# Kernel tuning notes

Hardware: AMD Instinct MI355X
Metric: run time of the kernel (lower is better)

Reference implementation:

```python
import jax, jax.numpy as jnp
import numpy as np

N, E, F_NODE, F_EDGE, EMB, HID, NGRAPH = 10000, 30000, 32, 8, 64, 16, 64


def _edge_mlp(e, w1, b1, w2, b2):
    # Seq(Linear(F_EDGE,16), ReLU, Linear(16, in*out))
    return jax.nn.relu(e @ w1 + b1) @ w2 + b2


def setup_inputs() -> dict:
    key = jax.random.key(0)
    ks = jax.random.split(key, 24)
    s = lambda k, shape, fan: jax.random.normal(k, shape, jnp.float32) * (1.0 / np.sqrt(fan))
    inp = {
        "x_p": jax.random.normal(ks[0], (N, F_NODE), jnp.float32),
        "x_d": jax.random.normal(ks[1], (1, F_NODE), jnp.float32),
        "edge_attr_p": jax.random.uniform(ks[2], (E, F_EDGE), jnp.float32),
        "edge_attr_d": jax.random.uniform(ks[3], (1, F_EDGE), jnp.float32),
        "edge_index_p": jax.random.randint(ks[4], (2, E), 0, N, jnp.int32),
        "x_p_batch": jnp.sort(jax.random.randint(ks[5], (N,), 0, NGRAPH, jnp.int32)),
        # edge MLP of first conv: F_EDGE -> 16 -> F_NODE*EMB
        "nn0_w1": s(ks[6], (F_EDGE, HID), F_EDGE), "nn0_b1": jnp.zeros((HID,), jnp.float32),
        "nn0_w2": s(ks[7], (HID, F_NODE * EMB), HID), "nn0_b2": jnp.zeros((F_NODE * EMB,), jnp.float32),
        # shared edge MLP of later convs: F_EDGE -> 16 -> EMB*EMB
        "nn1_w1": s(ks[8], (F_EDGE, HID), F_EDGE), "nn1_b1": jnp.zeros((HID,), jnp.float32),
        "nn1_w2": s(ks[9], (HID, EMB * EMB), HID), "nn1_b2": jnp.zeros((EMB * EMB,), jnp.float32),
        # per-conv root weights and biases
        "root0": s(ks[10], (F_NODE, EMB), F_NODE), "bias0": jnp.zeros((EMB,), jnp.float32),
        "root1": s(ks[11], (EMB, EMB), EMB), "bias1": jnp.zeros((EMB,), jnp.float32),
        "root2": s(ks[12], (EMB, EMB), EMB), "bias2": jnp.zeros((EMB,), jnp.float32),
        # head: Linear(EMB,EMB) then Linear(EMB,1), no activation between (per source)
        "lin0_w": s(ks[13], (EMB, EMB), EMB), "lin0_b": jnp.zeros((EMB,), jnp.float32),
        "lin1_w": s(ks[14], (EMB, 1), EMB), "lin1_b": jnp.zeros((1,), jnp.float32),
    }
    return inp


def reference(x_p, x_d, edge_attr_p, edge_attr_d,
              nn0_w1, nn0_b1, nn0_w2, nn0_b2,
              nn1_w1, nn1_b1, nn1_w2, nn1_b2,
              root0, bias0, root1, bias1, root2, bias2,
              lin0_w, lin0_b, lin1_w, lin1_b,
              edge_index_p, x_p_batch):
    src, dst = edge_index_p[0], edge_index_p[1]

    # conv 0: edge-conditioned weights [E, F_NODE, EMB]
    W0 = _edge_mlp(edge_attr_p, nn0_w1, nn0_b1, nn0_w2, nn0_b2).reshape(E, F_NODE, EMB)
    msg = jnp.einsum('ei,eio->eo', x_p[src], W0)
    agg = jax.ops.segment_sum(msg, dst, num_segments=N)
    x = jax.nn.relu(agg + x_p @ root0 + bias0)

    # convs 1..L-1 share the same edge MLP (same nn1 instance in source), so
    # the per-edge weight matrices [E, EMB, EMB] are identical: compute once.
    W1 = _edge_mlp(edge_attr_p, nn1_w1, nn1_b1, nn1_w2, nn1_b2).reshape(E, EMB, EMB)
    for root, bias in ((root1, bias1), (root2, bias2)):
        msg = jnp.einsum('ei,eio->eo', x[src], W1)
        agg = jax.ops.segment_sum(msg, dst, num_segments=N)
        x = jax.nn.relu(agg + x @ root + bias)

    # global max pool over graphs, dropout is identity in eval mode
    pooled = jax.ops.segment_max(x, x_p_batch, num_segments=NGRAPH)
    h = pooled @ lin0_w + lin0_b
    out = h @ lin1_w + lin1_b  # [NGRAPH, 1]
    return out
```

## Files before the change

kernel.cpp:

```cpp
#include <hip/hip_runtime.h>
#include <hip/hip_bf16.h>

#define N_NODES 10000
#define N_EDGES 30000
#define F_NODE  32
#define F_EDGE  8
#define EMB     64
#define HID     16
#define NGRAPH  64
#define NBUCK   625
#define CAP     128
#define NCOL    1088
#define ROWW    514

typedef __attribute__((ext_vector_type(8))) short short8;
typedef __attribute__((ext_vector_type(4))) float f32x4;

__device__ __forceinline__ unsigned short f2b(float f) {
    __hip_bfloat16 h = __float2bfloat16(f);
    return __builtin_bit_cast(unsigned short, h);
}

struct P {
    const float *x_p, *ea;
    const int *src, *dst, *batch;
    const float *nn0_w1, *nn0_b1, *nn0_w2, *nn0_b2;
    const float *nn1_w1, *nn1_b1, *nn1_w2, *nn1_b2;
    const float *root0, *bias0, *root1, *bias1, *root2, *bias2;
    const float *lin0_w, *lin0_b, *lin1_w, *lin1_b;
    float *out;
    int *cursor, *metap;
    float *A0p, *A1p;
    unsigned short *W2p0, *W2p1;
    float *AGGa, *AGGb, *X0, *X1, *POOL;
};

__global__ void __launch_bounds__(256) k_prep(P p) {
    int b = blockIdx.x, t = threadIdx.x;
    if (b < 118) {
        int e = b * 256 + t;
        if (e >= N_EDGES) return;
        float f[F_EDGE];
#pragma unroll
        for (int i = 0; i < F_EDGE; i++) f[i] = p.ea[e * F_EDGE + i];
        float a0[HID], a1[HID];
#pragma unroll
        for (int h = 0; h < HID; h++) {
            float s0 = p.nn0_b1[h], s1 = p.nn1_b1[h];
#pragma unroll
            for (int i = 0; i < F_EDGE; i++) {
                s0 += f[i] * p.nn0_w1[i * HID + h];
                s1 += f[i] * p.nn1_w1[i * HID + h];
            }
            a0[h] = fmaxf(s0, 0.f);
            a1[h] = fmaxf(s1, 0.f);
        }
        int s = p.src[e];
        int bk = s >> 4;
        int pos = atomicAdd(&p.cursor[bk], 1);
        if (pos < CAP) {
            size_t base = (size_t)bk * CAP + pos;
            p.metap[base] = p.dst[e] * 16 + (s & 15);
#pragma unroll
            for (int h = 0; h < HID; h++) {
                p.A0p[base * HID + h] = a0[h];
                p.A1p[base * HID + h] = a1[h];
            }
        }
    } else if (b < 254) {
        int i = (b - 118) * 256 + t;
        if (i >= NCOL * F_NODE) return;
        int rt = i >> 5, k = i & 31;
        float v;
        if (rt < 1024) {
            int T = rt >> 4, lr = rt & 15;
            int o = ((T >> 4) << 4) + lr, h = T & 15;
            v = p.nn0_w2[h * (F_NODE * EMB) + k * EMB + o];
        } else {
            v = p.nn0_b2[k * EMB + (rt - 1024)];
        }
        p.W2p0[i] = f2b(v);
    } else if (b < 526) {
        int i = (b - 254) * 256 + t;
        if (i >= NCOL * EMB) return;
        int rt = i >> 6, k = i & 63;
        float v;
        if (rt < 1024) {
            int T = rt >> 4, lr = rt & 15;
            int o = ((T >> 4) << 4) + lr, h = T & 15;
            v = p.nn1_w2[h * (EMB * EMB) + k * EMB + o];
        } else {
            v = p.nn1_b2[k * EMB + (rt - 1024)];
        }
        p.W2p1[i] = f2b(v);
    } else {
        int idx = (b - 526) * 256 + t;
        float4* Z = (float4*)p.AGGa;
        const float4 z4 = {0.f, 0.f, 0.f, 0.f};
        for (int i = idx; i < (N_NODES * EMB + NGRAPH * EMB) / 4; i += 160 * 256)
            Z[i] = z4;
    }
}

template <int CONV>
__global__ void __launch_bounds__(512) k_fused(P p) {
    constexpr int K = (CONV == 0) ? F_NODE : EMB;
    __shared__ unsigned short U2[16 * 2 * ROWW];
    __shared__ float XB_l[16][65];
    __shared__ float Xt[16][65];
    const int b = blockIdx.x, t = threadIdx.x;
    const int n0 = b * 16;
    const int w = t >> 6, l = t & 63;
    const int lrow = l & 15, lk4 = l >> 4;

    if (CONV == 0) {
        float4* Zb = (float4*)(p.AGGb + (size_t)n0 * EMB);
        const float4 z4 = {0.f, 0.f, 0.f, 0.f};
        for (int idx = t; idx < 16 * EMB / 4; idx += 512) Zb[idx] = z4;
    }

    if (CONV > 0) {
        const float* aggIn = (CONV == 1) ? p.AGGa : p.AGGb;
        const float* rt = (CONV == 1) ? p.root0 : p.root1;
        const float* bs = (CONV == 1) ? p.bias0 : p.bias1;
        constexpr int IN = (CONV == 1) ? F_NODE : EMB;
        for (int idx = t; idx < 16 * 64; idx += 512) {
            int j = idx >> 6, o = idx & 63;
            int n = n0 + j;
            float s = aggIn[n * EMB + o] + bs[o];
            const float* xr = (CONV == 1) ? (p.x_p + (size_t)n * IN)
                                          : (p.X0 + (size_t)n * IN);
#pragma unroll
            for (int i = 0; i < IN; i++) s += xr[i] * rt[i * EMB + o];
            float sv = fmaxf(s, 0.f);
            Xt[j][o] = sv;
            if (CONV == 1) { p.X0[n * EMB + o] = sv; p.AGGa[n * EMB + o] = 0.f; }
            else           { p.X1[n * EMB + o] = sv; }
        }
        __syncthreads();
    }

    short8 afr[K / 32];
    if (CONV == 0) {
        const float* xp = p.x_p + (size_t)(n0 + lrow) * F_NODE + lk4 * 8;
#pragma unroll
        for (int q = 0; q < 8; q++) afr[0][q] = (short)f2b(xp[q]);
    } else {
#pragma unroll
        for (int kk = 0; kk < K / 32; kk++)
#pragma unroll
            for (int q = 0; q < 8; q++)
                afr[kk][q] = (short)f2b(Xt[lrow][kk * 32 + lk4 * 8 + q]);
    }
    const unsigned short* W2p = (CONV == 0) ? p.W2p0 : p.W2p1;
    for (int i = 0; i <= 8; i++) {
        int T = w + 8 * i;
        if (T >= 68) break;
        short8 bfr[K / 32];
#pragma unroll
        for (int kk = 0; kk < K / 32; kk++)
            bfr[kk] = *reinterpret_cast<const short8*>(
                W2p + (size_t)(T * 16 + lrow) * K + kk * 32 + lk4 * 8);
        f32x4 acc = {0.f, 0.f, 0.f, 0.f};
#pragma unroll
        for (int kk = 0; kk < K / 32; kk++)
            acc = __builtin_amdgcn_mfma_f32_16x16x32_bf16(afr[kk], bfr[kk], acc, 0, 0, 0);
        if (T < 64) {
            int h = T & 15, hw = h >> 1, hb = h & 1;
            int ob = ((T >> 4) << 4) + lrow;
#pragma unroll
            for (int r = 0; r < 4; r++)
                U2[(lk4 * 4 + r) * (2 * ROWW) + hw * 128 + ob * 2 + hb] = f2b(acc[r]);
        } else {
            int col = (T - 64) * 16 + lrow;
#pragma unroll
            for (int r = 0; r < 4; r++)
                XB_l[lk4 * 4 + r][col] = acc[r];
        }
    }
    __syncthreads();

    const float* Ap = (CONV == 0) ? p.A0p : p.A1p;
    float* aggOut = (CONV == 1) ? p.AGGb : p.AGGa;
    int cnt = p.cursor[b];
    if (cnt > CAP) cnt = CAP;
    const size_t base = (size_t)b * CAP;
    const int o = l;
#pragma unroll 2
    for (int qi = w; qi < cnt; qi += 8) {
        int q = __builtin_amdgcn_readfirstlane(qi);
        int mt = p.metap[base + q];
        int sloc = mt & 15, dd = mt >> 4;
        const float* Ae = Ap + (base + q) * HID;
        float av[HID];
#pragma unroll
        for (int h = 0; h < HID; h++) av[h] = Ae[h];
        const unsigned* up = reinterpret_cast<const unsigned*>(U2) + sloc * ROWW + o;
        float m = XB_l[sloc][o];
#define ACC2(wrd, h)                                                              \
        m = fmaf(__builtin_bit_cast(float, (unsigned)(wrd) << 16), av[h], m);     \
        m = fmaf(__builtin_bit_cast(float, (unsigned)(wrd) & 0xffff0000u), av[h + 1], m);
#pragma unroll
        for (int hh = 0; hh < 8; hh++) {
            unsigned uw = up[hh * 64];
            ACC2(uw, 2 * hh)
        }
#undef ACC2
        atomicAdd(&aggOut[(size_t)dd * EMB + o], m);
    }
}

__global__ void __launch_bounds__(256) k_upd2(P p) {
    int w = threadIdx.x >> 6, o = threadIdx.x & 63;
    int n = __builtin_amdgcn_readfirstlane(blockIdx.x * 4 + w);
    float s = p.AGGa[n * EMB + o] + p.bias2[o];
    const float* xr = p.X1 + (size_t)n * EMB;
#pragma unroll
    for (int i = 0; i < EMB; i++) s += xr[i] * p.root2[i * EMB + o];
    s = fmaxf(s, 0.f);
    atomicMax((unsigned*)&p.POOL[p.batch[n] * EMB + o], __float_as_uint(s));
}

__global__ void k_head(P p) {
    int g = blockIdx.x, o2 = threadIdx.x;
    float h = p.lin0_b[o2];
    const float* Pg = p.POOL + g * EMB;
    for (int o = 0; o < EMB; o++) h += Pg[o] * p.lin0_w[o * EMB + o2];
    float v = h * p.lin1_w[o2];
#pragma unroll
    for (int off = 32; off; off >>= 1) v += __shfl_down(v, off, 64);
    if (o2 == 0) p.out[g] = v + p.lin1_b[0];
}

extern "C" void kernel_launch(void* const* d_in, const int* in_sizes, int n_in,
                              void* d_out, int out_size, void* d_ws, size_t ws_size,
                              hipStream_t stream) {
    P p;
    p.x_p    = (const float*)d_in[0];
    p.ea     = (const float*)d_in[2];
    const int* eidx = (const int*)d_in[4];
    p.src    = eidx;
    p.dst    = eidx + N_EDGES;
    p.batch  = (const int*)d_in[5];
    p.nn0_w1 = (const float*)d_in[6];  p.nn0_b1 = (const float*)d_in[7];
    p.nn0_w2 = (const float*)d_in[8];  p.nn0_b2 = (const float*)d_in[9];
    p.nn1_w1 = (const float*)d_in[10]; p.nn1_b1 = (const float*)d_in[11];
    p.nn1_w2 = (const float*)d_in[12]; p.nn1_b2 = (const float*)d_in[13];
    p.root0  = (const float*)d_in[14]; p.bias0  = (const float*)d_in[15];
    p.root1  = (const float*)d_in[16]; p.bias1  = (const float*)d_in[17];
    p.root2  = (const float*)d_in[18]; p.bias2  = (const float*)d_in[19];
    p.lin0_w = (const float*)d_in[20]; p.lin0_b = (const float*)d_in[21];
    p.lin1_w = (const float*)d_in[22]; p.lin1_b = (const float*)d_in[23];
    p.out    = (float*)d_out;

    char* ws = (char*)d_ws;
    p.cursor = (int*)ws;
    p.AGGa  = (float*)(ws + 4096);
    p.POOL  = p.AGGa + (size_t)N_NODES * EMB;
    p.AGGb  = p.POOL + (size_t)NGRAPH * EMB;
    char* w2 = (char*)(p.AGGb + (size_t)N_NODES * EMB);
    p.metap = (int*)w2;            w2 += (size_t)NBUCK * CAP * 4;
    p.A0p   = (float*)w2;          w2 += (size_t)NBUCK * CAP * HID * 4;
    p.A1p   = (float*)w2;          w2 += (size_t)NBUCK * CAP * HID * 4;
    p.W2p0  = (unsigned short*)w2; w2 += (size_t)NCOL * F_NODE * 2;
    p.W2p1  = (unsigned short*)w2; w2 += (size_t)NCOL * EMB * 2;
    p.X0    = (float*)w2;          w2 += (size_t)N_NODES * EMB * 4;
    p.X1    = (float*)w2;          w2 += (size_t)N_NODES * EMB * 4;

    hipMemsetAsync(p.cursor, 0, 4096, stream);
    k_prep<<<686, 256, 0, stream>>>(p);
    k_fused<0><<<NBUCK, 512, 0, stream>>>(p);
    k_fused<1><<<NBUCK, 512, 0, stream>>>(p);
    k_fused<2><<<NBUCK, 512, 0, stream>>>(p);
    k_upd2<<<2500, 256, 0, stream>>>(p);
    k_head<<<NGRAPH, 64, 0, stream>>>(p);
}
```

Measured before the change: 211.8 us.

## Move edge bucketing and edge-MLP first layer into conv0 blocks via LDS scan

Edge bucketing by source node is no longer done with global atomics in the prep kernel followed by a memset. Each conv0 block now scans the whole src array and collects its own edges with LDS atomics. The block computes both first-layer edge MLP activations for those edges. Conv0 activations stay in LDS, and only the conv1/2 activations and metadata go to global memory. This drops the memset, the global atomic contention and the A0 round trip, but every one of the 625 blocks now reads all 30000 src indices, which is redundant global traffic.

```diff
diff --git a/kernel.cpp b/kernel.cpp
--- a/kernel.cpp
+++ b/kernel.cpp
@@ -29,46 +29,16 @@
     const float *root0, *bias0, *root1, *bias1, *root2, *bias2;
     const float *lin0_w, *lin0_b, *lin1_w, *lin1_b;
     float *out;
-    int *cursor, *metap;
-    float *A0p, *A1p;
+    int *cnt, *metap;
+    float *A1p;
     unsigned short *W2p0, *W2p1;
     float *AGGa, *AGGb, *X0, *X1, *POOL;
 };
 
 __global__ void __launch_bounds__(256) k_prep(P p) {
     int b = blockIdx.x, t = threadIdx.x;
-    if (b < 118) {
-        int e = b * 256 + t;
-        if (e >= N_EDGES) return;
-        float f[F_EDGE];
-#pragma unroll
-        for (int i = 0; i < F_EDGE; i++) f[i] = p.ea[e * F_EDGE + i];
-        float a0[HID], a1[HID];
-#pragma unroll
-        for (int h = 0; h < HID; h++) {
-            float s0 = p.nn0_b1[h], s1 = p.nn1_b1[h];
-#pragma unroll
-            for (int i = 0; i < F_EDGE; i++) {
-                s0 += f[i] * p.nn0_w1[i * HID + h];
-                s1 += f[i] * p.nn1_w1[i * HID + h];
-            }
-            a0[h] = fmaxf(s0, 0.f);
-            a1[h] = fmaxf(s1, 0.f);
-        }
-        int s = p.src[e];
-        int bk = s >> 4;
-        int pos = atomicAdd(&p.cursor[bk], 1);
-        if (pos < CAP) {
-            size_t base = (size_t)bk * CAP + pos;
-            p.metap[base] = p.dst[e] * 16 + (s & 15);
-#pragma unroll
-            for (int h = 0; h < HID; h++) {
-                p.A0p[base * HID + h] = a0[h];
-                p.A1p[base * HID + h] = a1[h];
-            }
-        }
-    } else if (b < 254) {
-        int i = (b - 118) * 256 + t;
+    if (b < 136) {
+        int i = b * 256 + t;
         if (i >= NCOL * F_NODE) return;
         int rt = i >> 5, k = i & 31;
         float v;
@@ -80,8 +50,8 @@
             v = p.nn0_b2[k * EMB + (rt - 1024)];
         }
         p.W2p0[i] = f2b(v);
-    } else if (b < 526) {
-        int i = (b - 254) * 256 + t;
+    } else if (b < 408) {
+        int i = (b - 136) * 256 + t;
         if (i >= NCOL * EMB) return;
         int rt = i >> 6, k = i & 63;
         float v;
@@ -94,11 +64,11 @@
         }
         p.W2p1[i] = f2b(v);
     } else {
-        int idx = (b - 526) * 256 + t;
+        int idx = (b - 408) * 256 + t;
         float4* Z = (float4*)p.AGGa;
         const float4 z4 = {0.f, 0.f, 0.f, 0.f};
-        for (int i = idx; i < (N_NODES * EMB + NGRAPH * EMB) / 4; i += 160 * 256)
-            Z[i] = z4;
+        const int nv4 = (N_NODES * EMB + NGRAPH * EMB) / 4;
+        for (int i = idx; i < nv4; i += 160 * 256) Z[i] = z4;
     }
 }
 
@@ -108,15 +78,60 @@
     __shared__ unsigned short U2[16 * 2 * ROWW];
     __shared__ float XB_l[16][65];
     __shared__ float Xt[16][65];
+    __shared__ float A0l[CAP][HID];
+    __shared__ int lds_e[CAP];
+    __shared__ int meta_l[CAP];
+    __shared__ int lcnt;
     const int b = blockIdx.x, t = threadIdx.x;
     const int n0 = b * 16;
     const int w = t >> 6, l = t & 63;
     const int lrow = l & 15, lk4 = l >> 4;
+    int cnt = 0;
 
     if (CONV == 0) {
         float4* Zb = (float4*)(p.AGGb + (size_t)n0 * EMB);
         const float4 z4 = {0.f, 0.f, 0.f, 0.f};
         for (int idx = t; idx < 16 * EMB / 4; idx += 512) Zb[idx] = z4;
+        if (t == 0) lcnt = 0;
+        __syncthreads();
+        const int4* s4 = (const int4*)p.src;
+        for (int i = t; i < N_EDGES / 4; i += 512) {
+            int4 v = s4[i];
+            int e0 = i * 4;
+            if ((v.x >> 4) == b) { int sl = atomicAdd(&lcnt, 1); if (sl < CAP) lds_e[sl] = ((e0    ) << 4) | (v.x & 15); }
+            if ((v.y >> 4) == b) { int sl = atomicAdd(&lcnt, 1); if (sl < CAP) lds_e[sl] = ((e0 + 1) << 4) | (v.y & 15); }
+            if ((v.z >> 4) == b) { int sl = atomicAdd(&lcnt, 1); if (sl < CAP) lds_e[sl] = ((e0 + 2) << 4) | (v.z & 15); }
+            if ((v.w >> 4) == b) { int sl = atomicAdd(&lcnt, 1); if (sl < CAP) lds_e[sl] = ((e0 + 3) << 4) | (v.w & 15); }
+        }
+        __syncthreads();
+        cnt = lcnt; if (cnt > CAP) cnt = CAP;
+        if (t == 0) p.cnt[b] = cnt;
+        if (t < cnt) {
+            int pk = lds_e[t];
+            int e = pk >> 4, sloc = pk & 15;
+            int mt = p.dst[e] * 16 + sloc;
+            meta_l[t] = mt;
+            p.metap[(size_t)b * CAP + t] = mt;
+            const float4* ea4 = (const float4*)(p.ea + (size_t)e * F_EDGE);
+            float4 ef0 = ea4[0], ef1 = ea4[1];
+            float fv[F_EDGE] = {ef0.x, ef0.y, ef0.z, ef0.w, ef1.x, ef1.y, ef1.z, ef1.w};
+            float a1v[HID];
+#pragma unroll
+            for (int h = 0; h < HID; h++) {
+                float s0 = p.nn0_b1[h], s1 = p.nn1_b1[h];
+#pragma unroll
+                for (int i = 0; i < F_EDGE; i++) {
+                    s0 += fv[i] * p.nn0_w1[i * HID + h];
+                    s1 += fv[i] * p.nn1_w1[i * HID + h];
+                }
+                A0l[t][h] = fmaxf(s0, 0.f);
+                a1v[h] = fmaxf(s1, 0.f);
+            }
+            float4* A1g = (float4*)(p.A1p + ((size_t)b * CAP + t) * HID);
+#pragma unroll
+            for (int j = 0; j < 4; j++)
+                A1g[j] = float4{a1v[4 * j], a1v[4 * j + 1], a1v[4 * j + 2], a1v[4 * j + 3]};
+        }
     }
 
     if (CONV > 0) {
@@ -138,6 +153,7 @@
             else           { p.X1[n * EMB + o] = sv; }
         }
         __syncthreads();
+        cnt = p.cnt[b];
     }
 
     short8 afr[K / 32];
@@ -180,21 +196,29 @@
     }
     __syncthreads();
 
-    const float* Ap = (CONV == 0) ? p.A0p : p.A1p;
     float* aggOut = (CONV == 1) ? p.AGGb : p.AGGa;
-    int cnt = p.cursor[b];
-    if (cnt > CAP) cnt = CAP;
     const size_t base = (size_t)b * CAP;
     const int o = l;
 #pragma unroll 2
     for (int qi = w; qi < cnt; qi += 8) {
         int q = __builtin_amdgcn_readfirstlane(qi);
-        int mt = p.metap[base + q];
+        int mt;
+        float av[HID];
+        if (CONV == 0) {
+            mt = meta_l[q];
+            const float4* a4 = (const float4*)A0l[q];
+            float4 u0 = a4[0], u1 = a4[1], u2 = a4[2], u3 = a4[3];
+            av[0]=u0.x; av[1]=u0.y; av[2]=u0.z; av[3]=u0.w;
+            av[4]=u1.x; av[5]=u1.y; av[6]=u1.z; av[7]=u1.w;
+            av[8]=u2.x; av[9]=u2.y; av[10]=u2.z; av[11]=u2.w;
+            av[12]=u3.x; av[13]=u3.y; av[14]=u3.z; av[15]=u3.w;
+        } else {
+            mt = p.metap[base + q];
+            const float* Ae = p.A1p + (base + q) * HID;
+#pragma unroll
+            for (int h = 0; h < HID; h++) av[h] = Ae[h];
+        }
         int sloc = mt & 15, dd = mt >> 4;
-        const float* Ae = Ap + (base + q) * HID;
-        float av[HID];
-#pragma unroll
-        for (int h = 0; h < HID; h++) av[h] = Ae[h];
         const unsigned* up = reinterpret_cast<const unsigned*>(U2) + sloc * ROWW + o;
         float m = XB_l[sloc][o];
 #define ACC2(wrd, h)                                                              \
@@ -254,21 +278,19 @@
     p.out    = (float*)d_out;
 
     char* ws = (char*)d_ws;
-    p.cursor = (int*)ws;
-    p.AGGa  = (float*)(ws + 4096);
-    p.POOL  = p.AGGa + (size_t)N_NODES * EMB;
-    p.AGGb  = p.POOL + (size_t)NGRAPH * EMB;
-    char* w2 = (char*)(p.AGGb + (size_t)N_NODES * EMB);
-    p.metap = (int*)w2;            w2 += (size_t)NBUCK * CAP * 4;
-    p.A0p   = (float*)w2;          w2 += (size_t)NBUCK * CAP * HID * 4;
-    p.A1p   = (float*)w2;          w2 += (size_t)NBUCK * CAP * HID * 4;
-    p.W2p0  = (unsigned short*)w2; w2 += (size_t)NCOL * F_NODE * 2;
-    p.W2p1  = (unsigned short*)w2; w2 += (size_t)NCOL * EMB * 2;
-    p.X0    = (float*)w2;          w2 += (size_t)N_NODES * EMB * 4;
-    p.X1    = (float*)w2;          w2 += (size_t)N_NODES * EMB * 4;
-
-    hipMemsetAsync(p.cursor, 0, 4096, stream);
-    k_prep<<<686, 256, 0, stream>>>(p);
+    p.AGGa   = (float*)ws;
+    p.POOL   = p.AGGa + (size_t)N_NODES * EMB;
+    char* w2 = (char*)(p.POOL + (size_t)NGRAPH * EMB);
+    p.AGGb   = (float*)w2;          w2 += (size_t)N_NODES * EMB * 4;
+    p.cnt    = (int*)w2;            w2 += 2560;
+    p.metap  = (int*)w2;            w2 += (size_t)NBUCK * CAP * 4;
+    p.A1p    = (float*)w2;          w2 += (size_t)NBUCK * CAP * HID * 4;
+    p.W2p0   = (unsigned short*)w2; w2 += (size_t)NCOL * F_NODE * 2;
+    p.W2p1   = (unsigned short*)w2; w2 += (size_t)NCOL * EMB * 2;
+    p.X0     = (float*)w2;          w2 += (size_t)N_NODES * EMB * 4;
+    p.X1     = (float*)w2;          w2 += (size_t)N_NODES * EMB * 4;
+
+    k_prep<<<568, 256, 0, stream>>>(p);
     k_fused<0><<<NBUCK, 512, 0, stream>>>(p);
     k_fused<1><<<NBUCK, 512, 0, stream>>>(p);
     k_fused<2><<<NBUCK, 512, 0, stream>>>(p);
```

New measurement: 203.3 us. -4.0%, faster.
